# Optimization experiments

Measured on AMD Instinct MI355X. Metric: run time of the kernel, lower is better.

## Reference

```python
import jax, jax.numpy as jnp
import numpy as np

N_NODES = 100000
N_EDGES = 1600000
N_KEEP = 1280000  # int(N_EDGES * (1 - thr_a)), thr_a = 0.2
F_IN = 128
F_OUT = 128


def setup_inputs() -> dict:
    key = jax.random.key(0)
    ks = jax.random.split(key, 7)
    x = jax.random.normal(ks[0], (N_NODES, F_IN), dtype=jnp.float32)
    W = jax.random.normal(ks[1], (F_OUT, F_IN), dtype=jnp.float32) * (1.0 / np.sqrt(F_IN))
    bias = jax.random.normal(ks[2], (F_OUT,), dtype=jnp.float32)
    edge_src = jax.random.randint(ks[3], (N_EDGES,), 0, N_NODES, dtype=jnp.int32)
    edge_dst = jax.random.randint(ks[4], (N_EDGES,), 0, N_NODES, dtype=jnp.int32)
    edge_weight = jax.random.uniform(ks[5], (N_EDGES,), dtype=jnp.float32)
    idx_keep = jax.random.randint(ks[6], (N_KEEP,), 0, N_EDGES, dtype=jnp.int32)
    return {"x": x, "W": W, "bias": bias, "edge_src": edge_src,
            "edge_dst": edge_dst, "edge_weight": edge_weight, "idx_keep": idx_keep}


def reference(x, W, bias, edge_src, edge_dst, edge_weight, idx_keep):
    # Linear transform (pyg GCNConv lin has bias=False): h = x @ W.T  -> [N, F_out]
    h = jnp.einsum('nf,of->no', x, W)
    # Edge pruning: keep a random subset of edges (scheme_a='keep')
    src = edge_src[idx_keep]          # [M_keep]
    dst = edge_dst[idx_keep]          # [M_keep]
    ew = edge_weight[idx_keep]        # [M_keep]
    # propagate: message_j = h[src] * ew ; scatter-add into dst
    msg = h[src] * ew[:, None]        # [M_keep, F_out]
    out = jax.ops.segment_sum(msg, dst, num_segments=N_NODES)
    # GCNConv separate bias
    out = out + bias
    return out
```

## Files before the change

### kernel.cpp

```cpp
#include <hip/hip_runtime.h>

#define F 128
#define LDS_STRIDE 136
#define BUCKET 40

#define NPART 64
#define KE_SHIFT 15
#define PCAP1 27500
#define PCAP 22000
#define BIN_CAP 80
#define BIN_STRIDE 81
#define BIN2_CAP 48
#define BIN2_STRIDE 49
#define PA_CHUNK 2048
#define PB_CHUNK 1024
#define PB1_CHUNKS 27
#define PB_CHUNKS 22

typedef __attribute__((ext_vector_type(8))) short short8;
typedef __attribute__((ext_vector_type(4))) float floatx4;
typedef __attribute__((ext_vector_type(4))) float f32x4;

__device__ __forceinline__ unsigned short f32_to_bf16(float x) {
    unsigned u = __float_as_uint(x);
    unsigned r = u + 0x7FFFu + ((u >> 16) & 1u);
    return (unsigned short)(r >> 16);
}


__global__ __launch_bounds__(256, 2) void gemm_and_keybin(
    const float4* __restrict__ x4, const float4* __restrict__ W4,
    unsigned short* __restrict__ h2,
    int* __restrict__ cnt, int n_nodes,
    const int* __restrict__ idx_keep,
    unsigned* __restrict__ pair1, int* __restrict__ pair_cnt1,
    int m, int n_gemm_tiles, int n_part_chunks)
{
    __shared__ __align__(16) char smem[2 * 128 * LDS_STRIDE * 2];
    const int tid = threadIdx.x;
    const int bid = blockIdx.x;

    for (int i = bid * 256 + tid; i < n_nodes; i += gridDim.x * 256)
        cnt[i] = 0;

    const int r = bid % 9, c = bid / 9;

    if (r < 5) {
        const int tile = c * 5 + r;
        if (tile >= n_gemm_tiles) return;
        short* xs  = (short*)smem;
        short* wls = xs + 128 * LDS_STRIDE;
        const int node0 = tile * 128;

        for (int i = tid; i < 128 * 32; i += 256) {
            int row = i >> 5, c4 = i & 31;
            float4 v = W4[i];
            ushort4 b;
            b.x = f32_to_bf16(v.x); b.y = f32_to_bf16(v.y);
            b.z = f32_to_bf16(v.z); b.w = f32_to_bf16(v.w);
            *(ushort4*)&wls[row * LDS_STRIDE + c4 * 4] = b;
        }
        for (int i = tid; i < 128 * 32; i += 256) {
            int row = i >> 5, c4 = i & 31;
            int n = node0 + row;
            f32x4 v = (n < n_nodes)
                          ? __builtin_nontemporal_load((const f32x4*)&x4[(size_t)n * 32 + c4])
                          : (f32x4){0.f, 0.f, 0.f, 0.f};
            ushort4 b;
            b.x = f32_to_bf16(v[0]); b.y = f32_to_bf16(v[1]);
            b.z = f32_to_bf16(v[2]); b.w = f32_to_bf16(v[3]);
            *(ushort4*)&xs[row * LDS_STRIDE + c4 * 4] = b;
        }
        __syncthreads();

        const int wave = tid >> 6, lane = tid & 63;
        const int row16 = lane & 15, quad = lane >> 4;
        const int wrow0 = wave * 32;

        floatx4 acc[2][8];
        #pragma unroll
        for (int rr = 0; rr < 2; ++rr)
            #pragma unroll
            for (int cc = 0; cc < 8; ++cc)
                acc[rr][cc] = (floatx4){0.f, 0.f, 0.f, 0.f};

        #pragma unroll
        for (int s = 0; s < 4; ++s) {
            const int koff = s * 32 + quad * 8;
            short8 a[2];
            #pragma unroll
            for (int rr = 0; rr < 2; ++rr)
                a[rr] = *(const short8*)&xs[(wrow0 + rr * 16 + row16) * LDS_STRIDE + koff];
            #pragma unroll
            for (int cc = 0; cc < 8; ++cc) {
                short8 b = *(const short8*)&wls[(cc * 16 + row16) * LDS_STRIDE + koff];
                acc[0][cc] = __builtin_amdgcn_mfma_f32_16x16x32_bf16(a[0], b, acc[0][cc], 0, 0, 0);
                acc[1][cc] = __builtin_amdgcn_mfma_f32_16x16x32_bf16(a[1], b, acc[1][cc], 0, 0, 0);
            }
        }

        #pragma unroll
        for (int rr = 0; rr < 2; ++rr) {
            #pragma unroll
            for (int reg = 0; reg < 4; ++reg) {
                int n = node0 + wrow0 + rr * 16 + quad * 4 + reg;
                if (n < n_nodes) {
                    uint4 v;
                    v.x = (unsigned)f32_to_bf16(acc[rr][0][reg]) | ((unsigned)f32_to_bf16(acc[rr][1][reg]) << 16);
                    v.y = (unsigned)f32_to_bf16(acc[rr][2][reg]) | ((unsigned)f32_to_bf16(acc[rr][3][reg]) << 16);
                    v.z = (unsigned)f32_to_bf16(acc[rr][4][reg]) | ((unsigned)f32_to_bf16(acc[rr][5][reg]) << 16);
                    v.w = (unsigned)f32_to_bf16(acc[rr][6][reg]) | ((unsigned)f32_to_bf16(acc[rr][7][reg]) << 16);
                    *(uint4*)&h2[(size_t)n * F + row16 * 8] = v;
                }
            }
        }
    } else {
        const int chunk = c * 4 + (r - 5);
        if (chunk >= n_part_chunks) return;
        unsigned (*bins)[BIN_STRIDE] = (unsigned (*)[BIN_STRIDE])smem;
        int* bcnt  = (int*)(smem + NPART * BIN_STRIDE * 4);
        int* bbase = bcnt + NPART;

        for (int i = tid; i < NPART; i += 256) bcnt[i] = 0;
        __syncthreads();

        const int e0 = chunk * PA_CHUNK;
        #pragma unroll
        for (int k = 0; k < 2; ++k) {
            const int e_lin = e0 + (k * 256 + tid) * 4;
            int kes[4]; int nv = 0;
            if (e_lin + 3 < m) {
                int4 kv = *(const int4*)&idx_keep[e_lin];
                kes[0] = kv.x; kes[1] = kv.y; kes[2] = kv.z; kes[3] = kv.w; nv = 4;
            } else {
                for (int q = 0; q < 4; ++q)
                    if (e_lin + q < m) { kes[nv++] = idx_keep[e_lin + q]; }
            }
            for (int q = 0; q < nv; ++q) {
                unsigned ke = (unsigned)kes[q];
                int p = (int)(ke >> KE_SHIFT);
                int pos = atomicAdd(&bcnt[p], 1);
                if (pos < BIN_CAP) {
                    bins[p][pos] = ke;
                } else {
                    int g = atomicAdd(&pair_cnt1[p], 1);
                    if (g < PCAP1) pair1[(size_t)p * PCAP1 + g] = ke;
                }
            }
        }
        __syncthreads();

        for (int i = tid; i < NPART; i += 256) {
            int cc = min(bcnt[i], BIN_CAP);
            bbase[i] = atomicAdd(&pair_cnt1[i], cc);
        }
        __syncthreads();

        const int wave = tid >> 6, lane = tid & 63;
        for (int b = wave; b < NPART; b += 4) {
            int cc = min(bcnt[b], BIN_CAP);
            int base = bbase[b];
            for (int j = lane; j < cc; j += 64)
                if (base + j < PCAP1)
                    pair1[(size_t)b * PCAP1 + base + j] = bins[b][j];
        }
    }
}

__global__ __launch_bounds__(256) void resolve_bin(
    const unsigned* __restrict__ pair1, const int* __restrict__ pair_cnt1,
    const int* __restrict__ edge_src, const int* __restrict__ edge_dst,
    const float* __restrict__ edge_weight,
    unsigned short* __restrict__ bufDL, unsigned* __restrict__ bufPay,
    int* __restrict__ pair_cnt2, int npp)
{
    __shared__ unsigned long long bins[NPART][BIN2_STRIDE];
    __shared__ int bcnt[NPART];
    __shared__ int bbase[NPART];
    const int q = blockIdx.x % NPART;
    const int chunk = blockIdx.x / NPART;
    const int n = min(pair_cnt1[q], PCAP1);
    const int i0 = chunk * PB_CHUNK;
    if (i0 >= n) return;

    const int tid = threadIdx.x;
    for (int i = tid; i < NPART; i += 256) bcnt[i] = 0;
    __syncthreads();

    unsigned kes[4]; int idx[4];
    #pragma unroll
    for (int k = 0; k < 4; ++k) {
        idx[k] = i0 + k * 256 + tid;
        kes[k] = (idx[k] < n) ? pair1[(size_t)q * PCAP1 + idx[k]] : (unsigned)(q << KE_SHIFT);
    }
    int s[4], d[4]; float w[4];
    #pragma unroll
    for (int k = 0; k < 4; ++k) {
        s[k] = edge_src[kes[k]];
        d[k] = edge_dst[kes[k]];
        w[k] = edge_weight[kes[k]];
    }
    #pragma unroll
    for (int k = 0; k < 4; ++k) {
        if (idx[k] < n) {
            int p = d[k] / npp;
            int dl = d[k] - p * npp;
            unsigned w15 = (unsigned)__float2int_rn(w[k] * 32767.0f);
            unsigned pay = ((unsigned)s[k] << 15) | w15;
            unsigned long long entry = ((unsigned long long)dl << 32) | pay;
            int pos = atomicAdd(&bcnt[p], 1);
            if (pos < BIN2_CAP) {
                bins[p][pos] = entry;
            } else {
                int g = atomicAdd(&pair_cnt2[p], 1);
                if (g < PCAP) {
                    bufDL[(size_t)p * PCAP + g] = (unsigned short)dl;
                    bufPay[(size_t)p * PCAP + g] = pay;
                }
            }
        }
    }
    __syncthreads();

    for (int i = tid; i < NPART; i += 256) {
        int cc = min(bcnt[i], BIN2_CAP);
        bbase[i] = atomicAdd(&pair_cnt2[i], cc);
    }
    __syncthreads();

    const int wave = tid >> 6, lane = tid & 63;
    for (int b = wave; b < NPART; b += 4) {
        int cc = min(bcnt[b], BIN2_CAP);
        int base = bbase[b];
        for (int j = lane; j < cc; j += 64)
            if (base + j < PCAP) {
                unsigned long long e = bins[b][j];
                bufDL[(size_t)b * PCAP + base + j] = (unsigned short)(e >> 32);
                bufPay[(size_t)b * PCAP + base + j] = (unsigned)e;
            }
    }
}

__global__ __launch_bounds__(256) void fill_scatter(
    const unsigned short* __restrict__ bufDL, const unsigned* __restrict__ bufPay,
    const int* __restrict__ pair_cnt2,
    int* __restrict__ cnt, unsigned* __restrict__ perm, int npp)
{
    const int p = blockIdx.x % NPART;
    const int chunk = blockIdx.x / NPART;
    const int n = min(pair_cnt2[p], PCAP);
    const int i0 = chunk * PB_CHUNK;
    if (i0 >= n) return;

    int idx[4]; int dl[4]; unsigned pay[4];
    #pragma unroll
    for (int k = 0; k < 4; ++k) {
        idx[k] = i0 + k * 256 + threadIdx.x;
        int safe = (idx[k] < n) ? idx[k] : i0;
        dl[k] = bufDL[(size_t)p * PCAP + safe];
        pay[k] = bufPay[(size_t)p * PCAP + safe];
    }
    #pragma unroll
    for (int k = 0; k < 4; ++k) {
        if (idx[k] < n) {
            int d = p * npp + dl[k];
            int pos = atomicAdd(&cnt[d], 1);
            if (pos < BUCKET) perm[d * BUCKET + pos] = pay[k];
        }
    }
}

__global__ __launch_bounds__(256) void pull_wave(const unsigned* __restrict__ h4,
                                                 const int* __restrict__ cnt,
                                                 const unsigned* __restrict__ perm,
                                                 const float* __restrict__ bias,
                                                 float* __restrict__ out,
                                                 int n_nodes) {
    const int node = blockIdx.x * 4 + (threadIdx.x >> 6);
    const int lane = threadIdx.x & 63;
    if (node >= n_nodes) return;

    const int deg = min(cnt[node], BUCKET);

    int s = 0; float w = 0.0f;
    if (lane < deg) {
        unsigned entry = perm[node * BUCKET + lane];
        s = (int)(entry >> 15);
        w = (float)(entry & 0x7FFFu) * (1.0f / 32767.0f);
    }

    float acc0 = 0.0f, acc1 = 0.0f;
    for (int j = 0; j < deg; j += 4) {
        int sj[4]; float wj[4];
        #pragma unroll
        for (int q = 0; q < 4; ++q) {
            int jj = j + q;
            int take = (jj < deg) ? jj : 0;
            sj[q] = __shfl(s, take, 64);
            float t = __shfl(w, take, 64);
            wj[q] = (jj < deg) ? t : 0.0f;
        }
        unsigned hv[4];
        #pragma unroll
        for (int q = 0; q < 4; ++q)
            hv[q] = h4[(size_t)sj[q] * 64 + lane];
        #pragma unroll
        for (int q = 0; q < 4; ++q) {
            acc0 += __uint_as_float(hv[q] << 16) * wj[q];
            acc1 += __uint_as_float(hv[q] & 0xFFFF0000u) * wj[q];
        }
    }

    const int feat0 = 32 * (lane & 3) + (lane >> 2);
    const int feat1 = feat0 + 16;
    __builtin_nontemporal_store(acc0 + bias[feat0], &out[(size_t)node * F + feat0]);
    __builtin_nontemporal_store(acc1 + bias[feat1], &out[(size_t)node * F + feat1]);
}

extern "C" void kernel_launch(void* const* d_in, const int* in_sizes, int n_in,
                              void* d_out, int out_size, void* d_ws, size_t ws_size,
                              hipStream_t stream) {
    const float* x           = (const float*)d_in[0];
    const float* W           = (const float*)d_in[1];
    const float* bias        = (const float*)d_in[2];
    const int*   edge_src    = (const int*)d_in[3];
    const int*   edge_dst    = (const int*)d_in[4];
    const float* edge_weight = (const float*)d_in[5];
    const int*   idx_keep    = (const int*)d_in[6];
    float* out = (float*)d_out;

    const int n_nodes = in_sizes[0] / F;
    const int m_keep  = in_sizes[6];
    const int npp = (n_nodes + NPART - 1) / NPART;

    char* ws = (char*)d_ws;
    unsigned short* h2 = (unsigned short*)ws;
    size_t off = (size_t)n_nodes * F * 2;
    int* cnt = (int*)(ws + off);              off += (size_t)n_nodes * 4;
    int* pair_cnt1 = (int*)(ws + off);
    int* pair_cnt2 = (int*)(ws + off + 1024); off += 2048;
    unsigned short* bufDL = (unsigned short*)(ws + off); off += (size_t)NPART * PCAP * 2;
    unsigned* bufPay = (unsigned*)(ws + off); off += (size_t)NPART * PCAP * 4;
    unsigned* pair1 = (unsigned*)(ws + off);
    unsigned* perm  = (unsigned*)(ws + off);

    const int n_gemm_tiles  = (n_nodes + 127) / 128;
    const int n_part_chunks = (m_keep + PA_CHUNK - 1) / PA_CHUNK;
    const int gens = max((n_gemm_tiles + 4) / 5, (n_part_chunks + 3) / 4);
    const int grid = 9 * gens;

    hipMemsetAsync(pair_cnt1, 0, 2048, stream);

    gemm_and_keybin<<<grid, 256, 0, stream>>>(
        (const float4*)x, (const float4*)W, h2, cnt, n_nodes,
        idx_keep, pair1, pair_cnt1, m_keep, n_gemm_tiles, n_part_chunks);

    resolve_bin<<<NPART * PB1_CHUNKS, 256, 0, stream>>>(
        pair1, pair_cnt1, edge_src, edge_dst, edge_weight,
        bufDL, bufPay, pair_cnt2, npp);

    fill_scatter<<<NPART * PB_CHUNKS, 256, 0, stream>>>(
        bufDL, bufPay, pair_cnt2, cnt, perm, npp);

    pull_wave<<<(n_nodes + 3) / 4, 256, 0, stream>>>(
        (const unsigned*)h2, cnt, perm, bias, out, n_nodes);
}
```

Baseline: 275.4 us.

## Replace idx_keep binning with keep-count histogram and streaming edge pass

The old pipeline binned idx_keep values by edge partition and then gathered edge_src, edge_dst and edge_weight at random. The new one counts how many times each edge id is kept using global atomics, then streams all edge arrays in coalesced vectors and emits each kept edge once per count. The goal is to turn random gathers into sequential reads and drop the intermediate pair1 buffer. In exchange it adds a memset of the per-edge count array, 1.28M global atomics, and a pass over all edges rather than only the kept ones. The GEMM also moves out of the fused binning kernel into its own launch, so it no longer overlaps with the partition work.

```diff
diff --git a/kernel.cpp b/kernel.cpp
--- a/kernel.cpp
+++ b/kernel.cpp
@@ -5,16 +5,10 @@
 #define BUCKET 40
 
 #define NPART 64
-#define KE_SHIFT 15
-#define PCAP1 27500
 #define PCAP 22000
-#define BIN_CAP 80
-#define BIN_STRIDE 81
 #define BIN2_CAP 48
 #define BIN2_STRIDE 49
-#define PA_CHUNK 2048
 #define PB_CHUNK 1024
-#define PB1_CHUNKS 27
 #define PB_CHUNKS 22
 
 typedef __attribute__((ext_vector_type(8))) short short8;
@@ -28,194 +22,78 @@
 }
 
 
-__global__ __launch_bounds__(256, 2) void gemm_and_keybin(
-    const float4* __restrict__ x4, const float4* __restrict__ W4,
-    unsigned short* __restrict__ h2,
-    int* __restrict__ cnt, int n_nodes,
-    const int* __restrict__ idx_keep,
-    unsigned* __restrict__ pair1, int* __restrict__ pair_cnt1,
-    int m, int n_gemm_tiles, int n_part_chunks)
-{
-    __shared__ __align__(16) char smem[2 * 128 * LDS_STRIDE * 2];
-    const int tid = threadIdx.x;
-    const int bid = blockIdx.x;
-
-    for (int i = bid * 256 + tid; i < n_nodes; i += gridDim.x * 256)
-        cnt[i] = 0;
-
-    const int r = bid % 9, c = bid / 9;
-
-    if (r < 5) {
-        const int tile = c * 5 + r;
-        if (tile >= n_gemm_tiles) return;
-        short* xs  = (short*)smem;
-        short* wls = xs + 128 * LDS_STRIDE;
-        const int node0 = tile * 128;
-
-        for (int i = tid; i < 128 * 32; i += 256) {
-            int row = i >> 5, c4 = i & 31;
-            float4 v = W4[i];
-            ushort4 b;
-            b.x = f32_to_bf16(v.x); b.y = f32_to_bf16(v.y);
-            b.z = f32_to_bf16(v.z); b.w = f32_to_bf16(v.w);
-            *(ushort4*)&wls[row * LDS_STRIDE + c4 * 4] = b;
-        }
-        for (int i = tid; i < 128 * 32; i += 256) {
-            int row = i >> 5, c4 = i & 31;
-            int n = node0 + row;
-            f32x4 v = (n < n_nodes)
-                          ? __builtin_nontemporal_load((const f32x4*)&x4[(size_t)n * 32 + c4])
-                          : (f32x4){0.f, 0.f, 0.f, 0.f};
-            ushort4 b;
-            b.x = f32_to_bf16(v[0]); b.y = f32_to_bf16(v[1]);
-            b.z = f32_to_bf16(v[2]); b.w = f32_to_bf16(v[3]);
-            *(ushort4*)&xs[row * LDS_STRIDE + c4 * 4] = b;
-        }
-        __syncthreads();
-
-        const int wave = tid >> 6, lane = tid & 63;
-        const int row16 = lane & 15, quad = lane >> 4;
-        const int wrow0 = wave * 32;
-
-        floatx4 acc[2][8];
-        #pragma unroll
-        for (int rr = 0; rr < 2; ++rr)
-            #pragma unroll
-            for (int cc = 0; cc < 8; ++cc)
-                acc[rr][cc] = (floatx4){0.f, 0.f, 0.f, 0.f};
-
-        #pragma unroll
-        for (int s = 0; s < 4; ++s) {
-            const int koff = s * 32 + quad * 8;
-            short8 a[2];
-            #pragma unroll
-            for (int rr = 0; rr < 2; ++rr)
-                a[rr] = *(const short8*)&xs[(wrow0 + rr * 16 + row16) * LDS_STRIDE + koff];
-            #pragma unroll
-            for (int cc = 0; cc < 8; ++cc) {
-                short8 b = *(const short8*)&wls[(cc * 16 + row16) * LDS_STRIDE + koff];
-                acc[0][cc] = __builtin_amdgcn_mfma_f32_16x16x32_bf16(a[0], b, acc[0][cc], 0, 0, 0);
-                acc[1][cc] = __builtin_amdgcn_mfma_f32_16x16x32_bf16(a[1], b, acc[1][cc], 0, 0, 0);
-            }
-        }
-
-        #pragma unroll
-        for (int rr = 0; rr < 2; ++rr) {
-            #pragma unroll
-            for (int reg = 0; reg < 4; ++reg) {
-                int n = node0 + wrow0 + rr * 16 + quad * 4 + reg;
-                if (n < n_nodes) {
-                    uint4 v;
-                    v.x = (unsigned)f32_to_bf16(acc[rr][0][reg]) | ((unsigned)f32_to_bf16(acc[rr][1][reg]) << 16);
-                    v.y = (unsigned)f32_to_bf16(acc[rr][2][reg]) | ((unsigned)f32_to_bf16(acc[rr][3][reg]) << 16);
-                    v.z = (unsigned)f32_to_bf16(acc[rr][4][reg]) | ((unsigned)f32_to_bf16(acc[rr][5][reg]) << 16);
-                    v.w = (unsigned)f32_to_bf16(acc[rr][6][reg]) | ((unsigned)f32_to_bf16(acc[rr][7][reg]) << 16);
-                    *(uint4*)&h2[(size_t)n * F + row16 * 8] = v;
-                }
-            }
-        }
+__global__ __launch_bounds__(256) void histo_keep(const int* __restrict__ idx_keep,
+                                                  int* __restrict__ keep_cnt, int m) {
+    const int i = blockIdx.x * 256 + threadIdx.x;
+    const int base = i * 4;
+    if (base + 3 < m) {
+        int4 v = *(const int4*)&idx_keep[base];
+        atomicAdd(&keep_cnt[v.x], 1);
+        atomicAdd(&keep_cnt[v.y], 1);
+        atomicAdd(&keep_cnt[v.z], 1);
+        atomicAdd(&keep_cnt[v.w], 1);
     } else {
-        const int chunk = c * 4 + (r - 5);
-        if (chunk >= n_part_chunks) return;
-        unsigned (*bins)[BIN_STRIDE] = (unsigned (*)[BIN_STRIDE])smem;
-        int* bcnt  = (int*)(smem + NPART * BIN_STRIDE * 4);
-        int* bbase = bcnt + NPART;
-
-        for (int i = tid; i < NPART; i += 256) bcnt[i] = 0;
-        __syncthreads();
-
-        const int e0 = chunk * PA_CHUNK;
-        #pragma unroll
-        for (int k = 0; k < 2; ++k) {
-            const int e_lin = e0 + (k * 256 + tid) * 4;
-            int kes[4]; int nv = 0;
-            if (e_lin + 3 < m) {
-                int4 kv = *(const int4*)&idx_keep[e_lin];
-                kes[0] = kv.x; kes[1] = kv.y; kes[2] = kv.z; kes[3] = kv.w; nv = 4;
-            } else {
-                for (int q = 0; q < 4; ++q)
-                    if (e_lin + q < m) { kes[nv++] = idx_keep[e_lin + q]; }
-            }
-            for (int q = 0; q < nv; ++q) {
-                unsigned ke = (unsigned)kes[q];
-                int p = (int)(ke >> KE_SHIFT);
-                int pos = atomicAdd(&bcnt[p], 1);
-                if (pos < BIN_CAP) {
-                    bins[p][pos] = ke;
-                } else {
-                    int g = atomicAdd(&pair_cnt1[p], 1);
-                    if (g < PCAP1) pair1[(size_t)p * PCAP1 + g] = ke;
-                }
-            }
-        }
-        __syncthreads();
-
-        for (int i = tid; i < NPART; i += 256) {
-            int cc = min(bcnt[i], BIN_CAP);
-            bbase[i] = atomicAdd(&pair_cnt1[i], cc);
-        }
-        __syncthreads();
-
-        const int wave = tid >> 6, lane = tid & 63;
-        for (int b = wave; b < NPART; b += 4) {
-            int cc = min(bcnt[b], BIN_CAP);
-            int base = bbase[b];
-            for (int j = lane; j < cc; j += 64)
-                if (base + j < PCAP1)
-                    pair1[(size_t)b * PCAP1 + base + j] = bins[b][j];
-        }
-    }
-}
-
-__global__ __launch_bounds__(256) void resolve_bin(
-    const unsigned* __restrict__ pair1, const int* __restrict__ pair_cnt1,
+        for (int q = 0; q < 4; ++q)
+            if (base + q < m) atomicAdd(&keep_cnt[idx_keep[base + q]], 1);
+    }
+}
+
+__global__ __launch_bounds__(256) void resolve_stream(
     const int* __restrict__ edge_src, const int* __restrict__ edge_dst,
-    const float* __restrict__ edge_weight,
+    const float* __restrict__ edge_weight, const int* __restrict__ keep_cnt,
     unsigned short* __restrict__ bufDL, unsigned* __restrict__ bufPay,
-    int* __restrict__ pair_cnt2, int npp)
+    int* __restrict__ pair_cnt2, int n_edges, int npp)
 {
     __shared__ unsigned long long bins[NPART][BIN2_STRIDE];
     __shared__ int bcnt[NPART];
     __shared__ int bbase[NPART];
-    const int q = blockIdx.x % NPART;
-    const int chunk = blockIdx.x / NPART;
-    const int n = min(pair_cnt1[q], PCAP1);
-    const int i0 = chunk * PB_CHUNK;
-    if (i0 >= n) return;
-
     const int tid = threadIdx.x;
+
     for (int i = tid; i < NPART; i += 256) bcnt[i] = 0;
     __syncthreads();
 
-    unsigned kes[4]; int idx[4];
-    #pragma unroll
-    for (int k = 0; k < 4; ++k) {
-        idx[k] = i0 + k * 256 + tid;
-        kes[k] = (idx[k] < n) ? pair1[(size_t)q * PCAP1 + idx[k]] : (unsigned)(q << KE_SHIFT);
-    }
+    const int base = blockIdx.x * 1024 + tid * 4;
+    int kc[4] = {0, 0, 0, 0};
     int s[4], d[4]; float w[4];
-    #pragma unroll
-    for (int k = 0; k < 4; ++k) {
-        s[k] = edge_src[kes[k]];
-        d[k] = edge_dst[kes[k]];
-        w[k] = edge_weight[kes[k]];
-    }
-    #pragma unroll
-    for (int k = 0; k < 4; ++k) {
-        if (idx[k] < n) {
-            int p = d[k] / npp;
-            int dl = d[k] - p * npp;
-            unsigned w15 = (unsigned)__float2int_rn(w[k] * 32767.0f);
-            unsigned pay = ((unsigned)s[k] << 15) | w15;
+    if (base + 3 < n_edges) {
+        int4 kv = *(const int4*)&keep_cnt[base];
+        kc[0] = kv.x; kc[1] = kv.y; kc[2] = kv.z; kc[3] = kv.w;
+        int4 sv = *(const int4*)&edge_src[base];
+        s[0] = sv.x; s[1] = sv.y; s[2] = sv.z; s[3] = sv.w;
+        int4 dv = *(const int4*)&edge_dst[base];
+        d[0] = dv.x; d[1] = dv.y; d[2] = dv.z; d[3] = dv.w;
+        float4 wv = *(const float4*)&edge_weight[base];
+        w[0] = wv.x; w[1] = wv.y; w[2] = wv.z; w[3] = wv.w;
+    } else {
+        for (int q = 0; q < 4; ++q) {
+            if (base + q < n_edges) {
+                kc[q] = keep_cnt[base + q];
+                s[q] = edge_src[base + q];
+                d[q] = edge_dst[base + q];
+                w[q] = edge_weight[base + q];
+            }
+        }
+    }
+    #pragma unroll
+    for (int q = 0; q < 4; ++q) {
+        int k = min(kc[q], 32);
+        if (k > 0) {
+            int p = d[q] / npp;
+            int dl = d[q] - p * npp;
+            unsigned w15 = (unsigned)__float2int_rn(w[q] * 32767.0f);
+            unsigned pay = ((unsigned)s[q] << 15) | w15;
             unsigned long long entry = ((unsigned long long)dl << 32) | pay;
-            int pos = atomicAdd(&bcnt[p], 1);
-            if (pos < BIN2_CAP) {
-                bins[p][pos] = entry;
-            } else {
-                int g = atomicAdd(&pair_cnt2[p], 1);
-                if (g < PCAP) {
-                    bufDL[(size_t)p * PCAP + g] = (unsigned short)dl;
-                    bufPay[(size_t)p * PCAP + g] = pay;
+            int pos = atomicAdd(&bcnt[p], k);
+            for (int c = 0; c < k; ++c) {
+                int ps = pos + c;
+                if (ps < BIN2_CAP) {
+                    bins[p][ps] = entry;
+                } else {
+                    int g = atomicAdd(&pair_cnt2[p], 1);
+                    if (g < PCAP) {
+                        bufDL[(size_t)p * PCAP + g] = (unsigned short)dl;
+                        bufPay[(size_t)p * PCAP + g] = pay;
+                    }
                 }
             }
         }
@@ -231,12 +109,12 @@
     const int wave = tid >> 6, lane = tid & 63;
     for (int b = wave; b < NPART; b += 4) {
         int cc = min(bcnt[b], BIN2_CAP);
-        int base = bbase[b];
+        int base2 = bbase[b];
         for (int j = lane; j < cc; j += 64)
-            if (base + j < PCAP) {
+            if (base2 + j < PCAP) {
                 unsigned long long e = bins[b][j];
-                bufDL[(size_t)b * PCAP + base + j] = (unsigned short)(e >> 32);
-                bufPay[(size_t)b * PCAP + base + j] = (unsigned)e;
+                bufDL[(size_t)b * PCAP + base2 + j] = (unsigned short)(e >> 32);
+                bufPay[(size_t)b * PCAP + base2 + j] = (unsigned)e;
             }
     }
 }
@@ -266,6 +144,79 @@
             int d = p * npp + dl[k];
             int pos = atomicAdd(&cnt[d], 1);
             if (pos < BUCKET) perm[d * BUCKET + pos] = pay[k];
+        }
+    }
+}
+
+__global__ __launch_bounds__(256, 2) void gemm_mfma(const float4* __restrict__ x4,
+                                                    const float4* __restrict__ W4,
+                                                    unsigned short* __restrict__ h2,
+                                                    int n_nodes) {
+    __shared__ short xs[128 * LDS_STRIDE];
+    __shared__ short wls[128 * LDS_STRIDE];
+    const int tid = threadIdx.x;
+    const int node0 = blockIdx.x * 128;
+
+    for (int i = tid; i < 128 * 32; i += 256) {
+        int row = i >> 5, c4 = i & 31;
+        float4 v = W4[i];
+        ushort4 b;
+        b.x = f32_to_bf16(v.x); b.y = f32_to_bf16(v.y);
+        b.z = f32_to_bf16(v.z); b.w = f32_to_bf16(v.w);
+        *(ushort4*)&wls[row * LDS_STRIDE + c4 * 4] = b;
+    }
+    for (int i = tid; i < 128 * 32; i += 256) {
+        int row = i >> 5, c4 = i & 31;
+        int n = node0 + row;
+        f32x4 v = (n < n_nodes)
+                      ? __builtin_nontemporal_load((const f32x4*)&x4[(size_t)n * 32 + c4])
+                      : (f32x4){0.f, 0.f, 0.f, 0.f};
+        ushort4 b;
+        b.x = f32_to_bf16(v[0]); b.y = f32_to_bf16(v[1]);
+        b.z = f32_to_bf16(v[2]); b.w = f32_to_bf16(v[3]);
+        *(ushort4*)&xs[row * LDS_STRIDE + c4 * 4] = b;
+    }
+    __syncthreads();
+
+    const int wave = tid >> 6, lane = tid & 63;
+    const int row16 = lane & 15, quad = lane >> 4;
+    const int wrow0 = wave * 32;
+
+    floatx4 acc[2][8];
+    #pragma unroll
+    for (int rr = 0; rr < 2; ++rr)
+        #pragma unroll
+        for (int cc = 0; cc < 8; ++cc)
+            acc[rr][cc] = (floatx4){0.f, 0.f, 0.f, 0.f};
+
+    #pragma unroll
+    for (int s = 0; s < 4; ++s) {
+        const int koff = s * 32 + quad * 8;
+        short8 a[2];
+        #pragma unroll
+        for (int rr = 0; rr < 2; ++rr)
+            a[rr] = *(const short8*)&xs[(wrow0 + rr * 16 + row16) * LDS_STRIDE + koff];
+        #pragma unroll
+        for (int cc = 0; cc < 8; ++cc) {
+            short8 b = *(const short8*)&wls[(cc * 16 + row16) * LDS_STRIDE + koff];
+            acc[0][cc] = __builtin_amdgcn_mfma_f32_16x16x32_bf16(a[0], b, acc[0][cc], 0, 0, 0);
+            acc[1][cc] = __builtin_amdgcn_mfma_f32_16x16x32_bf16(a[1], b, acc[1][cc], 0, 0, 0);
+        }
+    }
+
+    #pragma unroll
+    for (int rr = 0; rr < 2; ++rr) {
+        #pragma unroll
+        for (int reg = 0; reg < 4; ++reg) {
+            int n = node0 + wrow0 + rr * 16 + quad * 4 + reg;
+            if (n < n_nodes) {
+                uint4 v;
+                v.x = (unsigned)f32_to_bf16(acc[rr][0][reg]) | ((unsigned)f32_to_bf16(acc[rr][1][reg]) << 16);
+                v.y = (unsigned)f32_to_bf16(acc[rr][2][reg]) | ((unsigned)f32_to_bf16(acc[rr][3][reg]) << 16);
+                v.z = (unsigned)f32_to_bf16(acc[rr][4][reg]) | ((unsigned)f32_to_bf16(acc[rr][5][reg]) << 16);
+                v.w = (unsigned)f32_to_bf16(acc[rr][6][reg]) | ((unsigned)f32_to_bf16(acc[rr][7][reg]) << 16);
+                *(uint4*)&h2[(size_t)n * F + row16 * 8] = v;
+            }
         }
     }
 }
@@ -330,6 +281,7 @@
     float* out = (float*)d_out;
 
     const int n_nodes = in_sizes[0] / F;
+    const int n_edges = in_sizes[3];
     const int m_keep  = in_sizes[6];
     const int npp = (n_nodes + NPART - 1) / NPART;
 
@@ -337,31 +289,27 @@
     unsigned short* h2 = (unsigned short*)ws;
     size_t off = (size_t)n_nodes * F * 2;
     int* cnt = (int*)(ws + off);              off += (size_t)n_nodes * 4;
-    int* pair_cnt1 = (int*)(ws + off);
-    int* pair_cnt2 = (int*)(ws + off + 1024); off += 2048;
+    int* pair_cnt2 = (int*)(ws + off);        off += 1024;
     unsigned short* bufDL = (unsigned short*)(ws + off); off += (size_t)NPART * PCAP * 2;
     unsigned* bufPay = (unsigned*)(ws + off); off += (size_t)NPART * PCAP * 4;
-    unsigned* pair1 = (unsigned*)(ws + off);
-    unsigned* perm  = (unsigned*)(ws + off);
-
-    const int n_gemm_tiles  = (n_nodes + 127) / 128;
-    const int n_part_chunks = (m_keep + PA_CHUNK - 1) / PA_CHUNK;
-    const int gens = max((n_gemm_tiles + 4) / 5, (n_part_chunks + 3) / 4);
-    const int grid = 9 * gens;
-
-    hipMemsetAsync(pair_cnt1, 0, 2048, stream);
-
-    gemm_and_keybin<<<grid, 256, 0, stream>>>(
-        (const float4*)x, (const float4*)W, h2, cnt, n_nodes,
-        idx_keep, pair1, pair_cnt1, m_keep, n_gemm_tiles, n_part_chunks);
-
-    resolve_bin<<<NPART * PB1_CHUNKS, 256, 0, stream>>>(
-        pair1, pair_cnt1, edge_src, edge_dst, edge_weight,
-        bufDL, bufPay, pair_cnt2, npp);
+    unsigned* perm = (unsigned*)(ws + off);
+    int* keep_cnt = (int*)(ws + off);
+
+    hipMemsetAsync(cnt, 0, (size_t)n_nodes * 4 + 1024, stream);
+    hipMemsetAsync(keep_cnt, 0, (size_t)n_edges * 4, stream);
+
+    histo_keep<<<(m_keep + 1023) / 1024, 256, 0, stream>>>(idx_keep, keep_cnt, m_keep);
+
+    resolve_stream<<<(n_edges + 1023) / 1024, 256, 0, stream>>>(
+        edge_src, edge_dst, edge_weight, keep_cnt,
+        bufDL, bufPay, pair_cnt2, n_edges, npp);
 
     fill_scatter<<<NPART * PB_CHUNKS, 256, 0, stream>>>(
         bufDL, bufPay, pair_cnt2, cnt, perm, npp);
 
+    gemm_mfma<<<(n_nodes + 127) / 128, 256, 0, stream>>>(
+        (const float4*)x, (const float4*)W, h2, n_nodes);
+
     pull_wave<<<(n_nodes + 3) / 4, 256, 0, stream>>>(
         (const unsigned*)h2, cnt, perm, bias, out, n_nodes);
 }
```

After: 325.0 us. 18.0% more time.
